# Performance work log

Measured on AMD Instinct MI355X. Metric: run time of the kernel, lower is better.

The kernel has to match this reference:

```python
import jax, jax.numpy as jnp
import numpy as np

B, S, H = 2, 2048, 1024
N_HEAD = 16
HEAD_DIM = H // N_HEAD


def setup_inputs() -> dict:
    key = jax.random.key(0)
    ks = jax.random.split(key, 8)
    init = 0.02
    return {
        "hidden_states": jax.random.normal(ks[0], (B, S, H), dtype=jnp.float32),
        "residual": jax.random.normal(ks[1], (B, S, H), dtype=jnp.float32),
        "alibi": jax.random.normal(ks[2], (B * N_HEAD, 1, S), dtype=jnp.float32),
        "attention_mask": jnp.ones((B, S), dtype=bool),
        "w_qkv": jax.random.normal(ks[3], (H, 3 * H), dtype=jnp.float32) * init,
        "b_qkv": jax.random.normal(ks[4], (3 * H,), dtype=jnp.float32) * init,
        "w_o": jax.random.normal(ks[5], (H, H), dtype=jnp.float32) * init,
        "b_o": jax.random.normal(ks[6], (H,), dtype=jnp.float32) * init,
        "layer_number": 4,
    }


def reference(hidden_states, residual, alibi, attention_mask, w_qkv, b_qkv, w_o, b_o, layer_number):
    b, s, h = hidden_states.shape
    nh, hd = N_HEAD, HEAD_DIM
    # fused QKV projection: (B,S,3H) -> (B,S,nh,3*hd) -> split
    fused_qkv = (hidden_states @ w_qkv + b_qkv).reshape(b, s, nh, 3 * hd)
    query, key, value = jnp.split(fused_qkv, 3, axis=-1)  # each (B,S,nh,hd)

    L = max(int(layer_number), 1)
    alpha = 1.0 / (np.sqrt(hd).astype(np.float32) * L)
    beta = 1.0 / L

    # scores = beta*alibi + alpha * q@k^T, reshaped to (B,nh,Sq,Sk)
    scores = jnp.einsum("bqnh,bknh->bnqk", query, key) * alpha
    scores = scores + beta * alibi.reshape(b, nh, 1, s)
    # FlaxBloomScaledSoftmax applies scale = layer_number before masking
    scores = scores * L

    # fused causal + padding mask (attention_mask_func): keep = causal & pad_q & pad_k
    causal = jnp.tril(jnp.ones((s, s), dtype=bool))
    pad = attention_mask  # (B,S) bool, True = attend
    keep = causal[None, None, :, :] & pad[:, None, :, None] & pad[:, None, None, :]  # (B,1,S,S)

    masked_scores = jnp.where(keep, scores, jnp.float32(-10000.0))
    probs = jax.nn.softmax(masked_scores.astype(jnp.float32), axis=-1) * keep
    probs = probs.astype(hidden_states.dtype)

    context = jnp.einsum("bnqk,bknh->bqnh", probs, value).reshape(b, s, h)
    attn_output = context @ w_o + b_o + residual
    return attn_output
```

## Files before the change

### kernel.cpp

```cpp
#include <hip/hip_runtime.h>
#include <hip/hip_bf16.h>

#define S_LEN 2048
#define HID   1024
#define NHEAD 16
#define HDIM  64
#define NBH   32

#define QSCALE 0.18033688f
#define LOG2E  1.44269504f

typedef __attribute__((ext_vector_type(8))) short short8;
typedef __attribute__((ext_vector_type(4))) float f32x4;

__device__ inline void gload_lds16(const void* g, void* l) {
  __builtin_amdgcn_global_load_lds(
      (const __attribute__((address_space(1))) void*)g,
      (__attribute__((address_space(3))) void*)l, 16, 0, 0);
}

__device__ inline ushort f2bf(float f) {
  __hip_bfloat16 h = __float2bfloat16(f);
  return *reinterpret_cast<const ushort*>(&h);
}

__device__ inline float exp2_fast(float x) {
  float r;
  asm("v_exp_f32 %0, %1" : "=v"(r) : "v"(x));
  return r;
}

__device__ inline void transpose_tile64(
    const float* __restrict__ in, ushort* __restrict__ out,
    int R, int C, int bx, int by, ushort (*Ls)[72])
{
    const int c0 = bx * 64, r0 = by * 64;
    const int t = threadIdx.x;
    const int tr = t >> 4, tc = (t & 15) * 4;
    #pragma unroll
    for (int i = 0; i < 4; ++i) {
        int gr = r0 + tr + i * 16;
        float4 v = *(const float4*)(in + (size_t)gr * C + c0 + tc);
        Ls[tc + 0][tr + i * 16] = f2bf(v.x);
        Ls[tc + 1][tr + i * 16] = f2bf(v.y);
        Ls[tc + 2][tr + i * 16] = f2bf(v.z);
        Ls[tc + 3][tr + i * 16] = f2bf(v.w);
    }
    __syncthreads();
    #pragma unroll
    for (int i = 0; i < 4; ++i) {
        int oc = c0 + tr + i * 16;
        ushort4 v = *(const ushort4*)&Ls[tr + i * 16][tc];
        *(ushort4*)(out + (size_t)oc * R + r0 + tc) = v;
    }
}

__global__ __launch_bounds__(256) void prep_fused(
    const float* __restrict__ X, ushort* __restrict__ Xb,
    const float* __restrict__ w_qkv, ushort* __restrict__ Wqkt,
    const float* __restrict__ w_o, ushort* __restrict__ Wot)
{
    __shared__ ushort Ls[64][72];
    const int b = blockIdx.x;
    if (b < 2048) {
        int i = b * 256 + threadIdx.x;
        float4 a = ((const float4*)X)[i * 2];
        float4 c = ((const float4*)X)[i * 2 + 1];
        union { ushort u[8]; uint4 v; } o;
        o.u[0]=f2bf(a.x); o.u[1]=f2bf(a.y); o.u[2]=f2bf(a.z); o.u[3]=f2bf(a.w);
        o.u[4]=f2bf(c.x); o.u[5]=f2bf(c.y); o.u[6]=f2bf(c.z); o.u[7]=f2bf(c.w);
        ((uint4*)Xb)[i] = o.v;
    } else if (b < 2816) {
        int t = b - 2048;
        transpose_tile64(w_qkv, Wqkt, 1024, 3072, t % 48, t / 48, Ls);
    } else {
        int t = b - 2816;
        transpose_tile64(w_o, Wot, 1024, 1024, t % 16, t / 16, Ls);
    }
}

__global__ __launch_bounds__(512, 2) void qkv_gemm_mfma(
    const ushort* __restrict__ A, const ushort* __restrict__ Bt,
    const float* __restrict__ bias,
    ushort* __restrict__ Q, ushort* __restrict__ K, ushort* __restrict__ V)
{
    __shared__ __align__(16) ushort As[2][256 * 64];
    __shared__ __align__(16) ushort Bs[2][192 * 64];
    const int tid = threadIdx.x;
    const int l   = tid & 63;
    const int w   = tid >> 6;
    const int wm  = w >> 2;
    const int wn  = w & 3;
    const int l7  = l & 7, l15 = l & 15, g = l >> 4;
    const int srow = l >> 3;
    const int schunk = l7 ^ srow;

    int lin = blockIdx.y * 16 + blockIdx.x;
    int swz = (lin & 7) * 32 + (lin >> 3);
    const int m0 = (swz >> 4) * 256;
    const int n0 = (swz & 15) * 192;

    f32x4 acc[8][3];
    #pragma unroll
    for (int i = 0; i < 8; ++i)
        #pragma unroll
        for (int j = 0; j < 3; ++j) acc[i][j] = (f32x4){0.f, 0.f, 0.f, 0.f};

#define STG_A(tt, qq) gload_lds16(A + (size_t)(m0 + (qq)*64 + w*8 + srow)*1024 \
                                    + (tt)*64 + schunk*8,                      \
                                  As[(tt) & 1] + ((qq)*64 + w*8)*64)
#define STG_B(tt, qq) gload_lds16(Bt + (size_t)(n0 + (qq)*64 + w*8 + srow)*1024 \
                                    + (tt)*64 + schunk*8,                       \
                                  Bs[(tt) & 1] + ((qq)*64 + w*8)*64)
#define LD_A(bb, mf, kk) (*(const short8*)(As[bb] + ((mf)*32 + wm*16 + l15)*64 \
                                           + ((((kk)*4 + g) ^ l7) << 3)))
#define LD_B(bb, nf, kk) (*(const short8*)(Bs[bb] + (wn*48 + (nf)*16 + l15)*64 \
                                           + ((((kk)*4 + g) ^ l7) << 3)))

    #pragma unroll
    for (int qq = 0; qq < 4; ++qq) STG_A(0, qq);
    #pragma unroll
    for (int qq = 0; qq < 3; ++qq) STG_B(0, qq);
    #pragma unroll
    for (int qq = 0; qq < 3; ++qq) { STG_A(1, qq); STG_B(1, qq); }
    asm volatile("s_waitcnt vmcnt(6)" ::: "memory");
    __builtin_amdgcn_s_barrier();

    short8 bfr[6];

    for (int it = 0; it < 8; ++it) {
        const int t = 2 * it;
        #pragma unroll
        for (int ph = 0; ph < 4; ++ph) {
            short8 afr[4];
            afr[0] = LD_A(0, 2*ph,     0);
            afr[1] = LD_A(0, 2*ph,     1);
            afr[2] = LD_A(0, 2*ph + 1, 0);
            afr[3] = LD_A(0, 2*ph + 1, 1);
            if (ph == 0) {
                #pragma unroll
                for (int nf = 0; nf < 3; ++nf) {
                    bfr[nf*2 + 0] = LD_B(0, nf, 0);
                    bfr[nf*2 + 1] = LD_B(0, nf, 1);
                }
            }
            if (ph == 0) { STG_A(t + 1, 3); }
            else if (t + 2 < 16) { STG_A(t + 2, ph - 1); STG_B(t + 2, ph - 1); }
            __builtin_amdgcn_s_barrier();
            asm volatile("s_waitcnt lgkmcnt(0)" ::: "memory");
            __builtin_amdgcn_sched_barrier(0);
            __builtin_amdgcn_s_setprio(1);
            #pragma unroll
            for (int kk = 0; kk < 2; ++kk)
                #pragma unroll
                for (int mi = 0; mi < 2; ++mi)
                    #pragma unroll
                    for (int nf = 0; nf < 3; ++nf)
                        acc[2*ph + mi][nf] = __builtin_amdgcn_mfma_f32_16x16x32_bf16(
                            afr[mi*2 + kk], bfr[nf*2 + kk], acc[2*ph + mi][nf], 0, 0, 0);
            __builtin_amdgcn_s_setprio(0);
            if (ph == 3) {
                if (it == 7) asm volatile("s_waitcnt vmcnt(0)" ::: "memory");
                else         asm volatile("s_waitcnt vmcnt(6)" ::: "memory");
            }
            __builtin_amdgcn_s_barrier();
        }
        #pragma unroll
        for (int ph = 0; ph < 4; ++ph) {
            short8 afr[4];
            afr[0] = LD_A(1, 2*ph,     0);
            afr[1] = LD_A(1, 2*ph,     1);
            afr[2] = LD_A(1, 2*ph + 1, 0);
            afr[3] = LD_A(1, 2*ph + 1, 1);
            if (ph == 0) {
                #pragma unroll
                for (int nf = 0; nf < 3; ++nf) {
                    bfr[nf*2 + 0] = LD_B(1, nf, 0);
                    bfr[nf*2 + 1] = LD_B(1, nf, 1);
                }
            }
            if (ph == 0) { if (t + 2 < 16) STG_A(t + 2, 3); }
            else if (t + 3 < 16) { STG_A(t + 3, ph - 1); STG_B(t + 3, ph - 1); }
            __builtin_amdgcn_s_barrier();
            asm volatile("s_waitcnt lgkmcnt(0)" ::: "memory");
            __builtin_amdgcn_sched_barrier(0);
            __builtin_amdgcn_s_setprio(1);
            #pragma unroll
            for (int kk = 0; kk < 2; ++kk)
                #pragma unroll
                for (int mi = 0; mi < 2; ++mi)
                    #pragma unroll
                    for (int nf = 0; nf < 3; ++nf)
                        acc[2*ph + mi][nf] = __builtin_amdgcn_mfma_f32_16x16x32_bf16(
                            afr[mi*2 + kk], bfr[nf*2 + kk], acc[2*ph + mi][nf], 0, 0, 0);
            __builtin_amdgcn_s_setprio(0);
            if (ph == 3) asm volatile("s_waitcnt vmcnt(6)" ::: "memory");
            __builtin_amdgcn_s_barrier();
        }
    }
#undef STG_A
#undef STG_B
#undef LD_A
#undef LD_B

    #pragma unroll
    for (int nf = 0; nf < 3; ++nf) {
        int gcol = n0 + wn * 48 + nf * 16 + l15;
        int head = gcol / 192;
        int rem  = gcol - head * 192;
        int which = rem >> 6;
        int d     = rem & 63;
        float bv = bias[gcol];
        #pragma unroll
        for (int mf = 0; mf < 8; ++mf) {
            int grow = m0 + mf * 32 + wm * 16 + g * 4;
            int bb = grow >> 11;
            int ss = grow & 2047;
            int bhh = (bb << 4) + head;
            if (which == 2) {
                ushort4 pk;
                pk.x = f2bf(acc[mf][nf][0] + bv);
                pk.y = f2bf(acc[mf][nf][1] + bv);
                pk.z = f2bf(acc[mf][nf][2] + bv);
                pk.w = f2bf(acc[mf][nf][3] + bv);
                *(ushort4*)(V + ((size_t)bhh * 64 + d) * S_LEN + ss) = pk;
            } else {
                ushort* plane = (which == 0) ? Q : K;
                float sc = (which == 0) ? QSCALE : 1.0f;
                ushort* dst = plane + (((size_t)bhh * S_LEN + ss) << 6) + d;
                #pragma unroll
                for (int r = 0; r < 4; ++r)
                    dst[(size_t)r << 6] = f2bf((acc[mf][nf][r] + bv) * sc);
            }
        }
    }
}

__global__ __launch_bounds__(512, 2) void out_gemm_mfma(
    const ushort* __restrict__ A, const ushort* __restrict__ Bt,
    const float* __restrict__ bias, const float* __restrict__ resid,
    float* __restrict__ out)
{
    __shared__ __align__(16) ushort As[2][256 * 64];
    __shared__ __align__(16) ushort Bs[2][64 * 64];
    const int tid = threadIdx.x;
    const int l   = tid & 63;
    const int w   = tid >> 6;
    const int wm  = w >> 2;
    const int wn  = w & 3;
    const int l7  = l & 7, l15 = l & 15, g = l >> 4;
    const int srow = l >> 3;
    const int schunk = l7 ^ srow;

    int lin = blockIdx.y * 16 + blockIdx.x;
    int swz = (lin & 7) * 32 + (lin >> 3);
    const int m0 = (swz >> 4) * 256;
    const int n0 = (swz & 15) * 64;

    f32x4 acc[8];
    #pragma unroll
    for (int i = 0; i < 8; ++i) acc[i] = (f32x4){0.f, 0.f, 0.f, 0.f};

#define OSTG_A(tt, qq) gload_lds16(A + (size_t)(m0 + (qq)*64 + w*8 + srow)*1024 \
                                     + (tt)*64 + schunk*8,                      \
                                   As[(tt) & 1] + ((qq)*64 + w*8)*64)
#define OSTG_B(tt)     gload_lds16(Bt + (size_t)(n0 + w*8 + srow)*1024          \
                                     + (tt)*64 + schunk*8,                      \
                                   Bs[(tt) & 1] + (w*8)*64)
#define OLD_A(bb, mf, kk) (*(const short8*)(As[bb] + ((mf)*32 + wm*16 + l15)*64 \
                                            + ((((kk)*4 + g) ^ l7) << 3)))
#define OLD_B(bb, kk)     (*(const short8*)(Bs[bb] + (wn*16 + l15)*64           \
                                            + ((((kk)*4 + g) ^ l7) << 3)))

    #pragma unroll
    for (int qq = 0; qq < 4; ++qq) OSTG_A(0, qq);
    OSTG_B(0);
    #pragma unroll
    for (int qq = 0; qq < 3; ++qq) OSTG_A(1, qq);
    OSTG_B(1);
    asm volatile("s_waitcnt vmcnt(4)" ::: "memory");
    __builtin_amdgcn_s_barrier();

    short8 bfr[2];

    for (int it = 0; it < 8; ++it) {
        const int t = 2 * it;
        #pragma unroll
        for (int ph = 0; ph < 4; ++ph) {
            short8 afr[4];
            afr[0] = OLD_A(0, 2*ph,     0);
            afr[1] = OLD_A(0, 2*ph,     1);
            afr[2] = OLD_A(0, 2*ph + 1, 0);
            afr[3] = OLD_A(0, 2*ph + 1, 1);
            if (ph == 0) { bfr[0] = OLD_B(0, 0); bfr[1] = OLD_B(0, 1); }
            if (ph == 0) { OSTG_A(t + 1, 3); }
            else if (t + 2 < 16) {
                OSTG_A(t + 2, ph - 1);
                if (ph == 1) OSTG_B(t + 2);
            }
            __builtin_amdgcn_s_barrier();
            asm volatile("s_waitcnt lgkmcnt(0)" ::: "memory");
            __builtin_amdgcn_sched_barrier(0);
            __builtin_amdgcn_s_setprio(1);
            #pragma unroll
            for (int kk = 0; kk < 2; ++kk)
                #pragma unroll
                for (int mi = 0; mi < 2; ++mi)
                    acc[2*ph + mi] = __builtin_amdgcn_mfma_f32_16x16x32_bf16(
                        afr[mi*2 + kk], bfr[kk], acc[2*ph + mi], 0, 0, 0);
            __builtin_amdgcn_s_setprio(0);
            if (ph == 3) {
                if (it == 7) asm volatile("s_waitcnt vmcnt(0)" ::: "memory");
                else         asm volatile("s_waitcnt vmcnt(4)" ::: "memory");
            }
            __builtin_amdgcn_s_barrier();
        }
        #pragma unroll
        for (int ph = 0; ph < 4; ++ph) {
            short8 afr[4];
            afr[0] = OLD_A(1, 2*ph,     0);
            afr[1] = OLD_A(1, 2*ph,     1);
            afr[2] = OLD_A(1, 2*ph + 1, 0);
            afr[3] = OLD_A(1, 2*ph + 1, 1);
            if (ph == 0) { bfr[0] = OLD_B(1, 0); bfr[1] = OLD_B(1, 1); }
            if (ph == 0) { if (t + 2 < 16) OSTG_A(t + 2, 3); }
            else if (t + 3 < 16) {
                OSTG_A(t + 3, ph - 1);
                if (ph == 1) OSTG_B(t + 3);
            }
            __builtin_amdgcn_s_barrier();
            asm volatile("s_waitcnt lgkmcnt(0)" ::: "memory");
            __builtin_amdgcn_sched_barrier(0);
            __builtin_amdgcn_s_setprio(1);
            #pragma unroll
            for (int kk = 0; kk < 2; ++kk)
                #pragma unroll
                for (int mi = 0; mi < 2; ++mi)
                    acc[2*ph + mi] = __builtin_amdgcn_mfma_f32_16x16x32_bf16(
                        afr[mi*2 + kk], bfr[kk], acc[2*ph + mi], 0, 0, 0);
            __builtin_amdgcn_s_setprio(0);
            if (ph == 3) asm volatile("s_waitcnt vmcnt(4)" ::: "memory");
            __builtin_amdgcn_s_barrier();
        }
    }
#undef OSTG_A
#undef OSTG_B
#undef OLD_A
#undef OLD_B

    {
        int gcol = n0 + wn * 16 + l15;
        float bv = bias[gcol];
        #pragma unroll
        for (int mf = 0; mf < 8; ++mf) {
            int grow = m0 + mf * 32 + wm * 16 + g * 4;
            #pragma unroll
            for (int r = 0; r < 4; ++r) {
                size_t idx = (size_t)(grow + r) * 1024 + gcol;
                out[idx] = acc[mf][r] + bv + resid[idx];
            }
        }
    }
}

#define STAGE(tt, idx) do {                                                   \
    gload_lds16(Kbh + (size_t)((tt) * 64 + w * 8 + srow) * 64 + schunk * 8,   \
                Ks[idx] + (w * 8) * 64);                                      \
    gload_lds16(Vbh + (size_t)(w * 8 + srow) * S_LEN + (tt) * 64 + schunk * 8,\
                Vs[idx] + (w * 8) * 64);                                      \
} while (0)

#define QK_TILE(SN, tt, idx, FULL) do {                                       \
    const ushort* Kc = Ks[idx];                                               \
    _Pragma("unroll")                                                         \
    for (int kb = 0; kb < 4; ++kb) {                                          \
        float4 a4 = *(const float4*)&alib[(tt) * 64 + kb * 16 + g * 4];       \
        SN[kb] = (f32x4){a4.x, a4.y, a4.z, a4.w};                             \
        if (FULL || (tt) * 64 + kb * 16 <= qmax) {                            \
            int row = kb * 16 + l15;                                          \
            short8 ka0 = *(const short8*)(Kc + row * 64 + ((g ^ l7) << 3));   \
            short8 ka1 = *(const short8*)(Kc + row * 64 + (((4+g) ^ l7) << 3));\
            SN[kb] = __builtin_amdgcn_mfma_f32_16x16x32_bf16(ka0, qb0, SN[kb], 0, 0, 0); \
            SN[kb] = __builtin_amdgcn_mfma_f32_16x16x32_bf16(ka1, qb1, SN[kb], 0, 0, 0); \
        }                                                                     \
    }                                                                         \
} while (0)

#define SM_PV(SC, tt, idx, FULL) do {                                         \
    const ushort* Vc = Vs[idx];                                               \
    ushort* Pw = Ps[w];                                                       \
    float p[16];                                                              \
    _Pragma("unroll")                                                         \
    for (int kb = 0; kb < 4; ++kb) {                                          \
        _Pragma("unroll")                                                     \
        for (int r = 0; r < 4; ++r) {                                         \
            float s = SC[kb][r];                                              \
            if (!FULL) {                                                      \
                int kglob = (tt) * 64 + kb * 16 + g * 4 + r;                  \
                s = (kglob > qglob) ? -1e30f : s;                             \
            }                                                                 \
            p[kb * 4 + r] = s;                                                \
        }                                                                     \
    }                                                                         \
    float mx0 = fmaxf(fmaxf(p[0], p[1]),   fmaxf(p[2], p[3]));                \
    float mx1 = fmaxf(fmaxf(p[4], p[5]),   fmaxf(p[6], p[7]));                \
    float mx2 = fmaxf(fmaxf(p[8], p[9]),   fmaxf(p[10], p[11]));              \
    float mx3 = fmaxf(fmaxf(p[12], p[13]), fmaxf(p[14], p[15]));              \
    float pmax = fmaxf(fmaxf(mx0, mx1), fmaxf(mx2, mx3));                     \
    pmax = fmaxf(pmax, __shfl_xor(pmax, 16));                                 \
    pmax = fmaxf(pmax, __shfl_xor(pmax, 32));                                 \
    if (!__all(pmax <= m + 11.5415603f)) {          \
        float mn = fmaxf(m, pmax);                                            \
        float resc = exp2_fast(m - mn);                                       \
        m = mn; lsum *= resc;                                                 \
        _Pragma("unroll")                                                     \
        for (int nb = 0; nb < 4; ++nb) oacc[nb] *= resc;                      \
    }                                                                         \
    _Pragma("unroll")                                                         \
    for (int i = 0; i < 16; ++i) p[i] = exp2_fast(p[i] - m);                  \
    float sm0 = (p[0] + p[1]) + (p[2] + p[3]);                                \
    float sm1 = (p[4] + p[5]) + (p[6] + p[7]);                                \
    float sm2 = (p[8] + p[9]) + (p[10] + p[11]);                              \
    float sm3 = (p[12] + p[13]) + (p[14] + p[15]);                            \
    float rsum = (sm0 + sm1) + (sm2 + sm3);                                   \
    rsum += __shfl_xor(rsum, 16);                                             \
    rsum += __shfl_xor(rsum, 32);                                             \
    lsum += rsum;                                                             \
    _Pragma("unroll")                                                         \
    for (int kb = 0; kb < 4; ++kb) {                                          \
        ushort4 pk;                                                           \
        pk.x = f2bf(p[kb * 4 + 0]); pk.y = f2bf(p[kb * 4 + 1]);               \
        pk.z = f2bf(p[kb * 4 + 2]); pk.w = f2bf(p[kb * 4 + 3]);               \
        int chunk = kb * 2 + (g >> 1);                                        \
        *(ushort4*)(Pw + l15 * 64 + ((chunk ^ l7) << 3) + ((g & 1) << 2)) = pk;\
    }                                                                         \
    short8 pb0 = *(const short8*)(Pw + l15 * 64 + ((g ^ l7) << 3));           \
    short8 pb1 = *(const short8*)(Pw + l15 * 64 + (((4 + g) ^ l7) << 3));     \
    _Pragma("unroll")                                                         \
    for (int nb = 0; nb < 4; ++nb) {                                          \
        int row = nb * 16 + l15;                                              \
        short8 va0 = *(const short8*)(Vc + row * 64 + ((g ^ l7) << 3));       \
        oacc[nb] = __builtin_amdgcn_mfma_f32_16x16x32_bf16(va0, pb0, oacc[nb], 0, 0, 0); \
    }                                                                         \
    if (FULL || (tt) * 64 + 32 <= qmax) {                                     \
        _Pragma("unroll")                                                     \
        for (int nb = 0; nb < 4; ++nb) {                                      \
            int row = nb * 16 + l15;                                          \
            short8 va1 = *(const short8*)(Vc + row * 64 + (((4 + g) ^ l7) << 3)); \
            oacc[nb] = __builtin_amdgcn_mfma_f32_16x16x32_bf16(va1, pb1, oacc[nb], 0, 0, 0); \
        }                                                                     \
    }                                                                         \
} while (0)

__global__ __launch_bounds__(512, 4) void attn_mfma(
    const ushort* __restrict__ Qp, const ushort* __restrict__ Kp,
    const ushort* __restrict__ Vtp, const float* __restrict__ alibi,
    ushort* __restrict__ ctx)
{
    __shared__ ushort Ks[3][64 * 64];
    __shared__ ushort Vs[3][64 * 64];
    __shared__ ushort Ps[8][16 * 64];
    __shared__ __align__(16) float alib[S_LEN];

    const int bh  = blockIdx.y;
    const int qt  = (blockIdx.y & 16) ? (int)blockIdx.x : 15 - (int)blockIdx.x;
    const int tid = threadIdx.x;
    const int w   = tid >> 6;
    const int l   = tid & 63;
    const int l7  = l & 7, l15 = l & 15, g = l >> 4;
    const int q0  = qt * 128;

    const ushort* Qbh = Qp  + (size_t)bh * S_LEN * HDIM;
    const ushort* Kbh = Kp  + (size_t)bh * S_LEN * HDIM;
    const ushort* Vbh = Vtp + (size_t)bh * HDIM * S_LEN;
    const float*  abh = alibi + (size_t)bh * S_LEN;

    const int qglob = q0 + w * 16 + l15;
    const int qmax  = q0 + w * 16 + 15;
    const int qmin  = q0 + w * 16;

    short8 qb0 = *(const short8*)(Qbh + (size_t)qglob * 64 + g * 8);
    short8 qb1 = *(const short8*)(Qbh + (size_t)qglob * 64 + 32 + g * 8);

    float m = -1e30f, lsum = 0.f;
    f32x4 oacc[4];
    #pragma unroll
    for (int nb = 0; nb < 4; ++nb) oacc[nb] = (f32x4){0.f, 0.f, 0.f, 0.f};

    const int srow   = l >> 3;
    const int schunk = (l & 7) ^ srow;

    {
        float4 a = *(const float4*)(abh + tid * 4);
        a.x *= LOG2E; a.y *= LOG2E; a.z *= LOG2E; a.w *= LOG2E;
        *(float4*)(alib + tid * 4) = a;
    }
    STAGE(0, 0);
    __syncthreads();
    STAGE(1, 1);

    f32x4 sa[4], sb[4];
    QK_TILE(sa, 0, 0, 0);

    const int nt = 2 * qt + 2;
    int ipv = 0, iqk = 1, ist = 2;
    for (int t = 0; t < nt; t += 2) {
        __syncthreads();
        if (t + 2 < nt) STAGE(t + 2, ist);
        if ((t + 1 < nt) && ((t + 1) * 64 + 63 <= qmin)) {
            QK_TILE(sb, t + 1, iqk, 1);
            SM_PV(sa, t, ipv, 1);
        } else {
            if ((t + 1 < nt) && ((t + 1) * 64 <= qmax)) QK_TILE(sb, t + 1, iqk, 0);
            if (t * 64 <= qmax) SM_PV(sa, t, ipv, 0);
        }
        { int tmp = ipv; ipv = iqk; iqk = ist; ist = tmp; }

        __syncthreads();
        if (t + 3 < nt) STAGE(t + 3, ist);
        if ((t + 2 < nt) && ((t + 2) * 64 + 63 <= qmin)) {
            QK_TILE(sa, t + 2, iqk, 1);
            SM_PV(sb, t + 1, ipv, 1);
        } else {
            if ((t + 2 < nt) && ((t + 2) * 64 <= qmax)) QK_TILE(sa, t + 2, iqk, 0);
            if ((t + 1) * 64 <= qmax) SM_PV(sb, t + 1, ipv, 0);
        }
        { int tmp = ipv; ipv = iqk; iqk = ist; ist = tmp; }
    }

    const int bb = bh >> 4, hh = bh & 15;
    float inv = 1.0f / lsum;
    ushort* crow = ctx + (size_t)(bb * S_LEN + qglob) * 1024 + hh * 64;
    #pragma unroll
    for (int nb = 0; nb < 4; ++nb) {
        ushort4 pk;
        pk.x = f2bf(oacc[nb][0] * inv);
        pk.y = f2bf(oacc[nb][1] * inv);
        pk.z = f2bf(oacc[nb][2] * inv);
        pk.w = f2bf(oacc[nb][3] * inv);
        *(ushort4*)(crow + nb * 16 + g * 4) = pk;
    }
}

extern "C" void kernel_launch(void* const* d_in, const int* in_sizes, int n_in,
                              void* d_out, int out_size, void* d_ws, size_t ws_size,
                              hipStream_t stream) {
    const float* X      = (const float*)d_in[0];
    const float* resid  = (const float*)d_in[1];
    const float* alibi  = (const float*)d_in[2];
    const float* w_qkv  = (const float*)d_in[4];
    const float* b_qkv  = (const float*)d_in[5];
    const float* w_o    = (const float*)d_in[6];
    const float* b_o    = (const float*)d_in[7];

    const size_t plane = (size_t)NBH * S_LEN * HDIM;
    ushort* Xb   = (ushort*)d_ws;
    ushort* Wqkt = Xb + (size_t)4096 * 1024;
    ushort* Wot  = Wqkt + (size_t)3072 * 1024;
    ushort* Qb   = Wot + (size_t)1024 * 1024;
    ushort* Kb   = Qb + plane;
    ushort* Vbt  = Qb + 2 * plane;
    ushort* ctx  = Qb + 3 * plane;
    float*  out  = (float*)d_out;

    prep_fused<<<3072, 256, 0, stream>>>(X, Xb, w_qkv, Wqkt, w_o, Wot);

    dim3 g1(3072 / 192, 4096 / 256);
    qkv_gemm_mfma<<<g1, 512, 0, stream>>>(Xb, Wqkt, b_qkv, Qb, Kb, Vbt);

    dim3 g2(S_LEN / 128, NBH);
    attn_mfma<<<g2, 512, 0, stream>>>(Qb, Kb, Vbt, alibi, ctx);

    dim3 g3(1024 / 64, 4096 / 256);
    out_gemm_mfma<<<g3, 512, 0, stream>>>(ctx, Wot, b_o, resid, out);
}
```

Measured before the change: 114.3 us.

## Restructure attention into single-wave blocks with direct global K/V loads

Rewrites the attention kernel so that each block is one 64-lane wave handling 32 query rows (two 16-row groups), instead of 8 waves sharing LDS-staged K/V tiles. K and V fragments are read straight from global memory, which drops the triple-buffered LDS staging and the block-wide barriers. Blocks are mapped so that each XCD works on the same heads, to improve L2 reuse, and heavy causal tiles are scheduled first. The cost is that LDS reuse of K/V across waves is lost, so there is more global/L2 traffic and the loads are unswizzled and uncoalesced. Alibi is also reloaded from global memory every tile.

```diff
diff --git a/kernel.cpp b/kernel.cpp
--- a/kernel.cpp
+++ b/kernel.cpp
@@ -363,45 +363,19 @@
     }
 }
 
-#define STAGE(tt, idx) do {                                                   \
-    gload_lds16(Kbh + (size_t)((tt) * 64 + w * 8 + srow) * 64 + schunk * 8,   \
-                Ks[idx] + (w * 8) * 64);                                      \
-    gload_lds16(Vbh + (size_t)(w * 8 + srow) * S_LEN + (tt) * 64 + schunk * 8,\
-                Vs[idx] + (w * 8) * 64);                                      \
-} while (0)
-
-#define QK_TILE(SN, tt, idx, FULL) do {                                       \
-    const ushort* Kc = Ks[idx];                                               \
-    _Pragma("unroll")                                                         \
-    for (int kb = 0; kb < 4; ++kb) {                                          \
-        float4 a4 = *(const float4*)&alib[(tt) * 64 + kb * 16 + g * 4];       \
-        SN[kb] = (f32x4){a4.x, a4.y, a4.z, a4.w};                             \
-        if (FULL || (tt) * 64 + kb * 16 <= qmax) {                            \
-            int row = kb * 16 + l15;                                          \
-            short8 ka0 = *(const short8*)(Kc + row * 64 + ((g ^ l7) << 3));   \
-            short8 ka1 = *(const short8*)(Kc + row * 64 + (((4+g) ^ l7) << 3));\
-            SN[kb] = __builtin_amdgcn_mfma_f32_16x16x32_bf16(ka0, qb0, SN[kb], 0, 0, 0); \
-            SN[kb] = __builtin_amdgcn_mfma_f32_16x16x32_bf16(ka1, qb1, SN[kb], 0, 0, 0); \
-        }                                                                     \
-    }                                                                         \
-} while (0)
-
-#define SM_PV(SC, tt, idx, FULL) do {                                         \
-    const ushort* Vc = Vs[idx];                                               \
-    ushort* Pw = Ps[w];                                                       \
+#define SOFTPACK(SC, m_, lsum_, oacc_, qlane, fullflag, grp) do {             \
     float p[16];                                                              \
     _Pragma("unroll")                                                         \
-    for (int kb = 0; kb < 4; ++kb) {                                          \
+    for (int kb = 0; kb < 4; ++kb)                                            \
         _Pragma("unroll")                                                     \
-        for (int r = 0; r < 4; ++r) {                                         \
-            float s = SC[kb][r];                                              \
-            if (!FULL) {                                                      \
-                int kglob = (tt) * 64 + kb * 16 + g * 4 + r;                  \
-                s = (kglob > qglob) ? -1e30f : s;                             \
+        for (int rr = 0; rr < 4; ++rr) {                                      \
+            float s = SC[kb][rr];                                             \
+            if (!(fullflag)) {                                                \
+                int kglob = t * 64 + kb * 16 + g * 4 + rr;                    \
+                s = (kglob > (qlane)) ? -1e30f : s;                           \
             }                                                                 \
-            p[kb * 4 + r] = s;                                                \
+            p[kb * 4 + rr] = s;                                               \
         }                                                                     \
-    }                                                                         \
     float mx0 = fmaxf(fmaxf(p[0], p[1]),   fmaxf(p[2], p[3]));                \
     float mx1 = fmaxf(fmaxf(p[4], p[5]),   fmaxf(p[6], p[7]));                \
     float mx2 = fmaxf(fmaxf(p[8], p[9]),   fmaxf(p[10], p[11]));              \
@@ -409,15 +383,15 @@
     float pmax = fmaxf(fmaxf(mx0, mx1), fmaxf(mx2, mx3));                     \
     pmax = fmaxf(pmax, __shfl_xor(pmax, 16));                                 \
     pmax = fmaxf(pmax, __shfl_xor(pmax, 32));                                 \
-    if (!__all(pmax <= m + 11.5415603f)) {          \
-        float mn = fmaxf(m, pmax);                                            \
-        float resc = exp2_fast(m - mn);                                       \
-        m = mn; lsum *= resc;                                                 \
+    if (!__all(pmax <= m_ + 11.5415603f)) {         \
+        float mn = fmaxf(m_, pmax);                                           \
+        float resc = exp2_fast(m_ - mn);                                      \
+        m_ = mn; lsum_ *= resc;                                               \
         _Pragma("unroll")                                                     \
-        for (int nb = 0; nb < 4; ++nb) oacc[nb] *= resc;                      \
+        for (int nb = 0; nb < 4; ++nb) oacc_[nb] *= resc;                     \
     }                                                                         \
     _Pragma("unroll")                                                         \
-    for (int i = 0; i < 16; ++i) p[i] = exp2_fast(p[i] - m);                  \
+    for (int i = 0; i < 16; ++i) p[i] = exp2_fast(p[i] - m_);                 \
     float sm0 = (p[0] + p[1]) + (p[2] + p[3]);                                \
     float sm1 = (p[4] + p[5]) + (p[6] + p[7]);                                \
     float sm2 = (p[8] + p[9]) + (p[10] + p[11]);                              \
@@ -425,120 +399,120 @@
     float rsum = (sm0 + sm1) + (sm2 + sm3);                                   \
     rsum += __shfl_xor(rsum, 16);                                             \
     rsum += __shfl_xor(rsum, 32);                                             \
-    lsum += rsum;                                                             \
+    lsum_ += rsum;                                                            \
     _Pragma("unroll")                                                         \
     for (int kb = 0; kb < 4; ++kb) {                                          \
         ushort4 pk;                                                           \
         pk.x = f2bf(p[kb * 4 + 0]); pk.y = f2bf(p[kb * 4 + 1]);               \
         pk.z = f2bf(p[kb * 4 + 2]); pk.w = f2bf(p[kb * 4 + 3]);               \
         int chunk = kb * 2 + (g >> 1);                                        \
-        *(ushort4*)(Pw + l15 * 64 + ((chunk ^ l7) << 3) + ((g & 1) << 2)) = pk;\
-    }                                                                         \
-    short8 pb0 = *(const short8*)(Pw + l15 * 64 + ((g ^ l7) << 3));           \
-    short8 pb1 = *(const short8*)(Pw + l15 * 64 + (((4 + g) ^ l7) << 3));     \
-    _Pragma("unroll")                                                         \
-    for (int nb = 0; nb < 4; ++nb) {                                          \
-        int row = nb * 16 + l15;                                              \
-        short8 va0 = *(const short8*)(Vc + row * 64 + ((g ^ l7) << 3));       \
-        oacc[nb] = __builtin_amdgcn_mfma_f32_16x16x32_bf16(va0, pb0, oacc[nb], 0, 0, 0); \
-    }                                                                         \
-    if (FULL || (tt) * 64 + 32 <= qmax) {                                     \
-        _Pragma("unroll")                                                     \
-        for (int nb = 0; nb < 4; ++nb) {                                      \
-            int row = nb * 16 + l15;                                          \
-            short8 va1 = *(const short8*)(Vc + row * 64 + (((4 + g) ^ l7) << 3)); \
-            oacc[nb] = __builtin_amdgcn_mfma_f32_16x16x32_bf16(va1, pb1, oacc[nb], 0, 0, 0); \
-        }                                                                     \
+        *(ushort4*)(Ps[grp] + l15 * 64 + ((chunk ^ l7) << 3) + ((g & 1) << 2)) = pk; \
     }                                                                         \
 } while (0)
 
-__global__ __launch_bounds__(512, 4) void attn_mfma(
+__global__ __launch_bounds__(64, 4) void attn_mfma(
     const ushort* __restrict__ Qp, const ushort* __restrict__ Kp,
     const ushort* __restrict__ Vtp, const float* __restrict__ alibi,
     ushort* __restrict__ ctx)
 {
-    __shared__ ushort Ks[3][64 * 64];
-    __shared__ ushort Vs[3][64 * 64];
-    __shared__ ushort Ps[8][16 * 64];
-    __shared__ __align__(16) float alib[S_LEN];
-
-    const int bh  = blockIdx.y;
-    const int qt  = (blockIdx.y & 16) ? (int)blockIdx.x : 15 - (int)blockIdx.x;
-    const int tid = threadIdx.x;
-    const int w   = tid >> 6;
-    const int l   = tid & 63;
+    __shared__ ushort Ps[2][16 * 64];
+
+    const int c   = blockIdx.x;
+    const int xcd = c & 7;
+    const int r   = c >> 3;
+    const int bh  = ((r & 3) << 3) | xcd;
+    const int qg  = 63 - (r >> 2);
+    const int l   = threadIdx.x;
     const int l7  = l & 7, l15 = l & 15, g = l >> 4;
-    const int q0  = qt * 128;
+    const int q0  = qg * 32;
 
     const ushort* Qbh = Qp  + (size_t)bh * S_LEN * HDIM;
     const ushort* Kbh = Kp  + (size_t)bh * S_LEN * HDIM;
     const ushort* Vbh = Vtp + (size_t)bh * HDIM * S_LEN;
     const float*  abh = alibi + (size_t)bh * S_LEN;
 
-    const int qglob = q0 + w * 16 + l15;
-    const int qmax  = q0 + w * 16 + 15;
-    const int qmin  = q0 + w * 16;
-
-    short8 qb0 = *(const short8*)(Qbh + (size_t)qglob * 64 + g * 8);
-    short8 qb1 = *(const short8*)(Qbh + (size_t)qglob * 64 + 32 + g * 8);
-
-    float m = -1e30f, lsum = 0.f;
-    f32x4 oacc[4];
-    #pragma unroll
-    for (int nb = 0; nb < 4; ++nb) oacc[nb] = (f32x4){0.f, 0.f, 0.f, 0.f};
-
-    const int srow   = l >> 3;
-    const int schunk = (l & 7) ^ srow;
-
-    {
-        float4 a = *(const float4*)(abh + tid * 4);
-        a.x *= LOG2E; a.y *= LOG2E; a.z *= LOG2E; a.w *= LOG2E;
-        *(float4*)(alib + tid * 4) = a;
-    }
-    STAGE(0, 0);
-    __syncthreads();
-    STAGE(1, 1);
-
-    f32x4 sa[4], sb[4];
-    QK_TILE(sa, 0, 0, 0);
-
-    const int nt = 2 * qt + 2;
-    int ipv = 0, iqk = 1, ist = 2;
-    for (int t = 0; t < nt; t += 2) {
-        __syncthreads();
-        if (t + 2 < nt) STAGE(t + 2, ist);
-        if ((t + 1 < nt) && ((t + 1) * 64 + 63 <= qmin)) {
-            QK_TILE(sb, t + 1, iqk, 1);
-            SM_PV(sa, t, ipv, 1);
-        } else {
-            if ((t + 1 < nt) && ((t + 1) * 64 <= qmax)) QK_TILE(sb, t + 1, iqk, 0);
-            if (t * 64 <= qmax) SM_PV(sa, t, ipv, 0);
-        }
-        { int tmp = ipv; ipv = iqk; iqk = ist; ist = tmp; }
-
-        __syncthreads();
-        if (t + 3 < nt) STAGE(t + 3, ist);
-        if ((t + 2 < nt) && ((t + 2) * 64 + 63 <= qmin)) {
-            QK_TILE(sa, t + 2, iqk, 1);
-            SM_PV(sb, t + 1, ipv, 1);
-        } else {
-            if ((t + 2 < nt) && ((t + 2) * 64 <= qmax)) QK_TILE(sa, t + 2, iqk, 0);
-            if ((t + 1) * 64 <= qmax) SM_PV(sb, t + 1, ipv, 0);
-        }
-        { int tmp = ipv; ipv = iqk; iqk = ist; ist = tmp; }
+    const int qa = q0 + l15;
+    const int qb = q0 + 16 + l15;
+    const int qmaxa = q0 + 15, qmaxb = q0 + 31;
+
+    short8 qfa0 = *(const short8*)(Qbh + (size_t)qa * 64 + g * 8);
+    short8 qfa1 = *(const short8*)(Qbh + (size_t)qa * 64 + 32 + g * 8);
+    short8 qfb0 = *(const short8*)(Qbh + (size_t)qb * 64 + g * 8);
+    short8 qfb1 = *(const short8*)(Qbh + (size_t)qb * 64 + 32 + g * 8);
+
+    float ma = -1e30f, la = 0.f, mb = -1e30f, lb = 0.f;
+    f32x4 oa[4], ob[4];
+    #pragma unroll
+    for (int nb = 0; nb < 4; ++nb) {
+        oa[nb] = (f32x4){0.f, 0.f, 0.f, 0.f};
+        ob[nb] = (f32x4){0.f, 0.f, 0.f, 0.f};
+    }
+
+    const int nt = (q0 + 31) / 64 + 1;
+    for (int t = 0; t < nt; ++t) {
+        const bool fulla = (t * 64 + 63 <= q0);
+        const bool fullb = (t * 64 + 63 <= q0 + 16);
+
+        f32x4 sa_[4], sb_[4];
+        #pragma unroll
+        for (int kb = 0; kb < 4; ++kb) {
+            float4 a4 = *(const float4*)(abh + t * 64 + kb * 16 + g * 4);
+            f32x4 ci = (f32x4){a4.x * LOG2E, a4.y * LOG2E,
+                               a4.z * LOG2E, a4.w * LOG2E};
+            sa_[kb] = ci; sb_[kb] = ci;
+            if (t * 64 + kb * 16 <= qmaxb) {
+                const ushort* kr = Kbh + (size_t)(t * 64 + kb * 16 + l15) * 64;
+                short8 ka0 = *(const short8*)(kr + g * 8);
+                short8 ka1 = *(const short8*)(kr + 32 + g * 8);
+                sb_[kb] = __builtin_amdgcn_mfma_f32_16x16x32_bf16(ka0, qfb0, sb_[kb], 0, 0, 0);
+                sb_[kb] = __builtin_amdgcn_mfma_f32_16x16x32_bf16(ka1, qfb1, sb_[kb], 0, 0, 0);
+                if (t * 64 + kb * 16 <= qmaxa) {
+                    sa_[kb] = __builtin_amdgcn_mfma_f32_16x16x32_bf16(ka0, qfa0, sa_[kb], 0, 0, 0);
+                    sa_[kb] = __builtin_amdgcn_mfma_f32_16x16x32_bf16(ka1, qfa1, sa_[kb], 0, 0, 0);
+                }
+            }
+        }
+
+        SOFTPACK(sa_, ma, la, oa, qa, fulla, 0);
+        SOFTPACK(sb_, mb, lb, ob, qb, fullb, 1);
+
+        short8 pa0 = *(const short8*)(Ps[0] + l15 * 64 + ((g ^ l7) << 3));
+        short8 pa1 = *(const short8*)(Ps[0] + l15 * 64 + (((4 + g) ^ l7) << 3));
+        short8 pb0 = *(const short8*)(Ps[1] + l15 * 64 + ((g ^ l7) << 3));
+        short8 pb1 = *(const short8*)(Ps[1] + l15 * 64 + (((4 + g) ^ l7) << 3));
+
+        #pragma unroll
+        for (int nb = 0; nb < 4; ++nb) {
+            const ushort* vr = Vbh + (size_t)(nb * 16 + l15) * S_LEN + t * 64;
+            short8 va0 = *(const short8*)(vr + g * 8);
+            oa[nb] = __builtin_amdgcn_mfma_f32_16x16x32_bf16(va0, pa0, oa[nb], 0, 0, 0);
+            ob[nb] = __builtin_amdgcn_mfma_f32_16x16x32_bf16(va0, pb0, ob[nb], 0, 0, 0);
+        }
+        if (t * 64 + 32 <= qmaxb) {
+            #pragma unroll
+            for (int nb = 0; nb < 4; ++nb) {
+                const ushort* vr = Vbh + (size_t)(nb * 16 + l15) * S_LEN + t * 64;
+                short8 va1 = *(const short8*)(vr + 32 + g * 8);
+                ob[nb] = __builtin_amdgcn_mfma_f32_16x16x32_bf16(va1, pb1, ob[nb], 0, 0, 0);
+                if (t * 64 + 32 <= qmaxa)
+                    oa[nb] = __builtin_amdgcn_mfma_f32_16x16x32_bf16(va1, pa1, oa[nb], 0, 0, 0);
+            }
+        }
     }
 
     const int bb = bh >> 4, hh = bh & 15;
-    float inv = 1.0f / lsum;
-    ushort* crow = ctx + (size_t)(bb * S_LEN + qglob) * 1024 + hh * 64;
+    float inva = 1.0f / la, invb = 1.0f / lb;
+    ushort* crowa = ctx + (size_t)(bb * S_LEN + qa) * 1024 + hh * 64;
+    ushort* crowb = ctx + (size_t)(bb * S_LEN + qb) * 1024 + hh * 64;
     #pragma unroll
     for (int nb = 0; nb < 4; ++nb) {
-        ushort4 pk;
-        pk.x = f2bf(oacc[nb][0] * inv);
-        pk.y = f2bf(oacc[nb][1] * inv);
-        pk.z = f2bf(oacc[nb][2] * inv);
-        pk.w = f2bf(oacc[nb][3] * inv);
-        *(ushort4*)(crow + nb * 16 + g * 4) = pk;
+        ushort4 pka, pkb;
+        pka.x = f2bf(oa[nb][0] * inva); pka.y = f2bf(oa[nb][1] * inva);
+        pka.z = f2bf(oa[nb][2] * inva); pka.w = f2bf(oa[nb][3] * inva);
+        pkb.x = f2bf(ob[nb][0] * invb); pkb.y = f2bf(ob[nb][1] * invb);
+        pkb.z = f2bf(ob[nb][2] * invb); pkb.w = f2bf(ob[nb][3] * invb);
+        *(ushort4*)(crowa + nb * 16 + g * 4) = pka;
+        *(ushort4*)(crowb + nb * 16 + g * 4) = pkb;
     }
 }
 
@@ -568,8 +542,7 @@
     dim3 g1(3072 / 192, 4096 / 256);
     qkv_gemm_mfma<<<g1, 512, 0, stream>>>(Xb, Wqkt, b_qkv, Qb, Kb, Vbt);
 
-    dim3 g2(S_LEN / 128, NBH);
-    attn_mfma<<<g2, 512, 0, stream>>>(Qb, Kb, Vbt, alibi, ctx);
+    attn_mfma<<<2048, 64, 0, stream>>>(Qb, Kb, Vbt, alibi, ctx);
 
     dim3 g3(1024 / 64, 4096 / 256);
     out_gemm_mfma<<<g3, 512, 0, stream>>>(ctx, Wot, b_o, resid, out);
```

Measured after the change: 205.1 us. +79.5%, slower.
